# Performance work log

Measured on AMD Instinct MI355X. Metric: run time of the kernel, lower is better.

## Reference

```python
import jax, jax.numpy as jnp
import numpy as np

N_NODES = 100000
N_EDGES = 600000
D_IN = 128
D_OUT = 128


def setup_inputs() -> dict:
    key = jax.random.key(0)
    k1, k2, k3 = jax.random.split(key, 3)
    x = jax.random.normal(k1, (N_NODES, D_IN), dtype=jnp.float32)
    edge_index = jax.random.randint(k2, (2, N_EDGES), 0, N_NODES, dtype=jnp.int64)
    # Glorot-style init for the GCN weight, zero bias (PyG defaults)
    W = jax.random.normal(k3, (D_IN, D_OUT), dtype=jnp.float32) * (1.0 / np.sqrt(D_IN))
    b = jnp.zeros((D_OUT,), dtype=jnp.float32)
    return {"x": x, "edge_index": edge_index, "W": W, "b": b}


def reference(x, edge_index, W, b):
    """GCNConv: out = D^{-1/2} (A + I) D^{-1/2} (x @ W) + b."""
    n = x.shape[0]
    self_loop = jnp.arange(n, dtype=edge_index.dtype)
    src = jnp.concatenate([edge_index[0], self_loop])  # [E + N]
    dst = jnp.concatenate([edge_index[1], self_loop])

    xw = x @ W  # [N, D_OUT] dense transform before aggregation

    # symmetric normalization with self-loops
    deg = jax.ops.segment_sum(jnp.ones_like(dst, dtype=x.dtype), dst, num_segments=n)
    dinv = jnp.where(deg > 0, jax.lax.rsqrt(deg), 0.0)
    norm = dinv[src] * dinv[dst]  # [E + N]

    # gather source features, scale, scatter-add to destinations
    msgs = norm[:, None] * xw[src]  # [E + N, D_OUT]
    out = jax.ops.segment_sum(msgs, dst, num_segments=n)
    return out + b
```

## Files before the change

kernel.cpp:

```cpp
#include <hip/hip_runtime.h>
#include <hip/hip_bf16.h>
#include <stdint.h>

#define N_NODES 100000
#define N_EDGES 600000
#define D 128
#define SCAN_NBLK ((N_NODES + 255) / 256)
#define CAP 32

typedef unsigned short u16;
typedef uint32_t u32;
typedef __attribute__((ext_vector_type(8))) short bf16x8;
typedef __attribute__((ext_vector_type(4))) float f32x4;

union bfpack { bf16x8 v; u16 s[8]; };

__device__ __forceinline__ float bf2f(u16 u) {
    union { u32 i; float f; } v; v.i = ((u32)u) << 16; return v.f;
}
__device__ __forceinline__ u16 f2bf(float f) {
    union { float f; u32 i; } v; v.f = f;
    u32 lsb = (v.i >> 16) & 1u;
    return (u16)((v.i + 0x7fffu + lsb) >> 16);
}

__global__ __launch_bounds__(256) void k_init(const u32* __restrict__ xu,
                                              const int* __restrict__ ei,
                                              int* __restrict__ deg,
                                              int* __restrict__ flags) {
    int t = threadIdx.x;
    int idx = blockIdx.x * 256 + t;
    if (idx < N_NODES) deg[idx] = 0;
    if (blockIdx.x == 0) {
        __shared__ int cnt[2];
        if (t < 2) cnt[t] = 0;
        __syncthreads();
        const u32* eu = (const u32*)ei;
        int bad = 0, zc = 0;
        for (int i = 0; i < 16; i++) {
            u32 w = xu[t + 256 * i];
            int e0 = (w >> 7) & 0xFF, e1 = (w >> 23) & 0xFF;
            bad += ((e0 == 0 || e0 == 0xFF) ? 1 : 0) + ((e1 == 0 || e1 == 0xFF) ? 1 : 0);
            zc += (eu[2 * (t + 256 * i) + 1] == 0) ? 1 : 0;
        }
        atomicAdd(&cnt[0], bad);
        atomicAdd(&cnt[1], zc);
        __syncthreads();
        if (t == 0) { flags[0] = cnt[0] > 8 ? 1 : 0; flags[1] = cnt[1] > 2048 ? 1 : 0; }
    }
}

__global__ __launch_bounds__(256) void k_prep(const int* __restrict__ flags,
                                              const void* __restrict__ Wp,
                                              u16* __restrict__ wthi,
                                              u16* __restrict__ wtlo) {
    int t = blockIdx.x * 256 + threadIdx.x;
    if (flags[0]) {
        const float* Wf = (const float*)Wp;
        for (int i = 0; i < 8; i++) {
            int idx = t + i * 2048;
            float w = Wf[idx];
            int k = idx >> 7, n = idx & 127;
            u16 h = f2bf(w);
            wthi[n * 128 + k] = h;
            wtlo[n * 128 + k] = f2bf(w - bf2f(h));
        }
    } else {
        const u16* W16 = (const u16*)Wp;
        for (int i = 0; i < 8; i++) {
            int idx = t + i * 2048;
            int k = idx >> 7, n = idx & 127;
            wthi[n * 128 + k] = W16[idx];
        }
    }
}

__global__ __launch_bounds__(256) void k_build(const int* __restrict__ ei,
                                               const int* __restrict__ flags,
                                               int* __restrict__ cnt,
                                               int* __restrict__ csr) {
    int e = blockIdx.x * 256 + threadIdx.x;
    if (e >= N_EDGES) return;
    int s, d;
    if (flags[1]) { s = ei[2 * e]; d = ei[2 * (N_EDGES + e)]; }
    else          { s = ei[e];     d = ei[N_EDGES + e]; }
    if ((unsigned)s >= N_NODES) s = 0;
    if ((unsigned)d >= N_NODES) d = 0;
    int slot = atomicAdd(&cnt[d], 1);
    if (slot < CAP) csr[(long)d * CAP + slot] = s;
}

__global__ void k_hist(const int* __restrict__ ei, const int* __restrict__ flags,
                       int* __restrict__ deg) {
    int e = blockIdx.x * 256 + threadIdx.x;
    if (e < N_EDGES) {
        int d = flags[1] ? ei[2 * (N_EDGES + e)] : ei[N_EDGES + e];
        if ((unsigned)d >= N_NODES) d = 0;
        atomicAdd(&deg[d], 1);
    }
}

__global__ __launch_bounds__(256) void k_reduce(const int* __restrict__ deg,
                                                int* __restrict__ bsum) {
    __shared__ int ws[4];
    int t = threadIdx.x, lane = t & 63, wave = t >> 6;
    int idx = blockIdx.x * 256 + t;
    int v = (idx < N_NODES) ? deg[idx] : 0;
    for (int o = 32; o > 0; o >>= 1) v += __shfl_down(v, o, 64);
    if (lane == 0) ws[wave] = v;
    __syncthreads();
    if (t == 0) bsum[blockIdx.x] = ws[0] + ws[1] + ws[2] + ws[3];
}

__global__ __launch_bounds__(512) void k_scanbs(const int* __restrict__ bsum,
                                                int* __restrict__ bpre,
                                                int* __restrict__ offs) {
    __shared__ int lds[512];
    int t = threadIdx.x;
    int v = (t < SCAN_NBLK) ? bsum[t] : 0;
    lds[t] = v;
    __syncthreads();
    for (int off = 1; off < 512; off <<= 1) {
        int u = (t >= off) ? lds[t - off] : 0;
        __syncthreads();
        lds[t] += u;
        __syncthreads();
    }
    if (t < SCAN_NBLK) bpre[t] = (t == 0) ? 0 : lds[t - 1];
    if (t == SCAN_NBLK - 1) offs[N_NODES] = lds[t];
}

__global__ __launch_bounds__(256) void k_apply(const int* __restrict__ deg,
                                               const int* __restrict__ bpre,
                                               int* __restrict__ offs,
                                               int* __restrict__ cursor) {
    __shared__ int ws[4];
    int t = threadIdx.x, lane = t & 63, wave = t >> 6;
    int idx = blockIdx.x * 256 + t;
    int d = (idx < N_NODES) ? deg[idx] : 0;
    int v = d;
    for (int o = 1; o < 64; o <<= 1) {
        int u = __shfl_up(v, o, 64);
        if (lane >= o) v += u;
    }
    if (lane == 63) ws[wave] = v;
    __syncthreads();
    int add = 0;
    for (int w = 0; w < wave; w++) add += ws[w];
    int excl = bpre[blockIdx.x] + add + v - d;
    if (idx < N_NODES) {
        offs[idx] = excl;
        cursor[idx] = excl;
    }
}

__global__ void k_scatter(const int* __restrict__ ei, const int* __restrict__ flags,
                          int* __restrict__ cursor, int* __restrict__ csr) {
    int e = blockIdx.x * 256 + threadIdx.x;
    if (e < N_EDGES) {
        int s, d;
        if (flags[1]) { s = ei[2 * e]; d = ei[2 * (N_EDGES + e)]; }
        else          { s = ei[e];     d = ei[N_EDGES + e]; }
        if ((unsigned)s >= N_NODES) s = 0;
        if ((unsigned)d >= N_NODES) d = 0;
        int slot = atomicAdd(&cursor[d], 1);
        csr[slot] = s;
    }
}

__global__ __launch_bounds__(256, 2) void k_gemm(const int* __restrict__ flags,
                                                 const void* __restrict__ xp,
                                                 const u16* __restrict__ wthi,
                                                 const u16* __restrict__ wtlo,
                                                 const int* __restrict__ deg,
                                                 u16* __restrict__ xw) {
    int t = threadIdx.x, wave = t >> 6, lane = t & 63;
    int m16 = lane & 15, q = lane >> 4;
    int row0 = blockIdx.x * 128 + wave * 32;
    f32x4 acc[2][8];
    for (int a = 0; a < 2; a++)
        for (int c = 0; c < 8; c++) acc[a][c] = (f32x4){0.f, 0.f, 0.f, 0.f};

    int r0 = row0 + m16;      if (r0 > N_NODES - 1) r0 = N_NODES - 1;
    int r1 = row0 + 16 + m16; if (r1 > N_NODES - 1) r1 = N_NODES - 1;

    if (flags[0]) {
        const float* xf = (const float*)xp;
        for (int kt = 0; kt < 4; kt++) {
            int kbase = kt * 32 + q * 8;
            float4 u0 = *(const float4*)(xf + (long)r0 * D + kbase);
            float4 u1 = *(const float4*)(xf + (long)r0 * D + kbase + 4);
            float4 v0 = *(const float4*)(xf + (long)r1 * D + kbase);
            float4 v1 = *(const float4*)(xf + (long)r1 * D + kbase + 4);
            float t0[8] = {u0.x, u0.y, u0.z, u0.w, u1.x, u1.y, u1.z, u1.w};
            float t1[8] = {v0.x, v0.y, v0.z, v0.w, v1.x, v1.y, v1.z, v1.w};
            bfpack h0, l0, h1, l1;
            for (int j = 0; j < 8; j++) {
                u16 a = f2bf(t0[j]); h0.s[j] = a; l0.s[j] = f2bf(t0[j] - bf2f(a));
                u16 b = f2bf(t1[j]); h1.s[j] = b; l1.s[j] = f2bf(t1[j] - bf2f(b));
            }
            for (int ct = 0; ct < 8; ct++) {
                bf16x8 bh = *(const bf16x8*)(wthi + (ct * 16 + m16) * 128 + kbase);
                bf16x8 bl = *(const bf16x8*)(wtlo + (ct * 16 + m16) * 128 + kbase);
                acc[0][ct] = __builtin_amdgcn_mfma_f32_16x16x32_bf16(h0.v, bh, acc[0][ct], 0, 0, 0);
                acc[0][ct] = __builtin_amdgcn_mfma_f32_16x16x32_bf16(l0.v, bh, acc[0][ct], 0, 0, 0);
                acc[0][ct] = __builtin_amdgcn_mfma_f32_16x16x32_bf16(h0.v, bl, acc[0][ct], 0, 0, 0);
                acc[1][ct] = __builtin_amdgcn_mfma_f32_16x16x32_bf16(h1.v, bh, acc[1][ct], 0, 0, 0);
                acc[1][ct] = __builtin_amdgcn_mfma_f32_16x16x32_bf16(l1.v, bh, acc[1][ct], 0, 0, 0);
                acc[1][ct] = __builtin_amdgcn_mfma_f32_16x16x32_bf16(h1.v, bl, acc[1][ct], 0, 0, 0);
            }
        }
    } else {
        const u16* x16 = (const u16*)xp;
        bf16x8 wb[8][4];
#pragma unroll
        for (int ct = 0; ct < 8; ct++)
#pragma unroll
            for (int kt = 0; kt < 4; kt++)
                wb[ct][kt] = *(const bf16x8*)(wthi + (ct * 16 + m16) * 128 + kt * 32 + q * 8);
        bf16x8 a0[4], a1[4];
#pragma unroll
        for (int kt = 0; kt < 4; kt++) {
            int kbase = kt * 32 + q * 8;
            a0[kt] = *(const bf16x8*)(x16 + (long)r0 * D + kbase);
            a1[kt] = *(const bf16x8*)(x16 + (long)r1 * D + kbase);
        }
#pragma unroll
        for (int kt = 0; kt < 4; kt++)
#pragma unroll
            for (int ct = 0; ct < 8; ct++) {
                acc[0][ct] = __builtin_amdgcn_mfma_f32_16x16x32_bf16(a0[kt], wb[ct][kt], acc[0][ct], 0, 0, 0);
                acc[1][ct] = __builtin_amdgcn_mfma_f32_16x16x32_bf16(a1[kt], wb[ct][kt], acc[1][ct], 0, 0, 0);
            }
    }
    for (int a = 0; a < 2; a++)
        for (int r = 0; r < 4; r++) {
            int row = row0 + a * 16 + q * 4 + r;
            if (row < N_NODES) {
                float dr = rsqrtf((float)(deg[row] + 1));
                for (int ct = 0; ct < 8; ct++)
                    xw[(long)row * D + ct * 16 + m16] = f2bf(dr * acc[a][ct][r]);
            }
        }
}

__global__ __launch_bounds__(256) void k_agg_bkt(const int* __restrict__ flags,
                                                 const u16* __restrict__ xw,
                                                 const int* __restrict__ csr,
                                                 const int* __restrict__ cnt,
                                                 const void* __restrict__ bp,
                                                 void* __restrict__ outp) {
    int t = threadIdx.x;
    int wave = t >> 6, lane = t & 63;
    int g = lane >> 4, i = lane & 15;
    int nb = blockIdx.x * 16 + wave * 4;
    int n = nb + g;

    int4 dv = *(const int4*)(cnt + nb);
    int deg = (g == 0) ? dv.x : (g == 1) ? dv.y : (g == 2) ? dv.z : dv.w;
    float dn = rsqrtf((float)(deg + 1));
    int m = deg < CAP ? deg : CAP;
    int rounds = (m + 3) >> 2;
    float padf = (float)(1 - (rounds * 4 - m));

    const u16* xwc = xw + i * 8;
    bfpack pv; pv.v = *(const bf16x8*)(xwc + (long)n * D);
    float ax[8];
#pragma unroll
    for (int j2 = 0; j2 < 8; j2++) ax[j2] = bf2f(pv.s[j2]) * padf;

    const int* base = csr + (long)n * CAP;
    for (int j = 0; j < m; j += 4) {
        int4 qi = *(const int4*)(base + j);
        int s0 = qi.x;
        int s1 = (j + 1 < m) ? qi.y : n;
        int s2 = (j + 2 < m) ? qi.z : n;
        int s3 = (j + 3 < m) ? qi.w : n;
        bfpack g0, g1, g2, g3;
        g0.v = *(const bf16x8*)(xwc + (long)s0 * D);
        g1.v = *(const bf16x8*)(xwc + (long)s1 * D);
        g2.v = *(const bf16x8*)(xwc + (long)s2 * D);
        g3.v = *(const bf16x8*)(xwc + (long)s3 * D);
#pragma unroll
        for (int j2 = 0; j2 < 8; j2++)
            ax[j2] += (bf2f(g0.s[j2]) + bf2f(g1.s[j2])) +
                      (bf2f(g2.s[j2]) + bf2f(g3.s[j2]));
    }

    if (flags[0]) {
        const float* bf_ = (const float*)bp;
        f32x4 b0 = *(const f32x4*)(bf_ + i * 8);
        f32x4 b1 = *(const f32x4*)(bf_ + i * 8 + 4);
        f32x4 o0, o1;
#pragma unroll
        for (int j2 = 0; j2 < 4; j2++) {
            o0[j2] = dn * ax[j2] + b0[j2];
            o1[j2] = dn * ax[j2 + 4] + b1[j2];
        }
        float* outf = (float*)outp;
        *(f32x4*)(outf + (long)n * D + i * 8) = o0;
        *(f32x4*)(outf + (long)n * D + i * 8 + 4) = o1;
    } else {
        const u16* b16 = (const u16*)bp;
        bfpack bb; bb.v = *(const bf16x8*)(b16 + i * 8);
        bfpack ob;
#pragma unroll
        for (int j2 = 0; j2 < 8; j2++) ob.s[j2] = f2bf(dn * ax[j2] + bf2f(bb.s[j2]));
        u16* out16 = (u16*)outp;
        *(bf16x8*)(out16 + (long)n * D + i * 8) = ob.v;
    }
}

__global__ __launch_bounds__(256) void k_agg_csr(const int* __restrict__ flags,
                                                 const u16* __restrict__ xw,
                                                 const int* __restrict__ csr,
                                                 const int* __restrict__ offs,
                                                 const void* __restrict__ bp,
                                                 void* __restrict__ outp) {
    int wave = threadIdx.x >> 6, lane = threadIdx.x & 63;
    int n = blockIdx.x * 4 + wave;
    int c = lane * 2;
    int e0 = offs[n], e1 = offs[n + 1];
    float dn = rsqrtf((float)(e1 - e0 + 1));
    u32 pv = *(const u32*)(xw + (long)n * D + c);
    float ax = bf2f((u16)pv), ay = bf2f((u16)(pv >> 16));
    int j = e0;
    for (; j + 4 <= e1; j += 4) {
        int s0 = csr[j], s1 = csr[j + 1], s2 = csr[j + 2], s3 = csr[j + 3];
        u32 q0 = *(const u32*)(xw + (long)s0 * D + c);
        u32 q1 = *(const u32*)(xw + (long)s1 * D + c);
        u32 q2 = *(const u32*)(xw + (long)s2 * D + c);
        u32 q3 = *(const u32*)(xw + (long)s3 * D + c);
        ax += bf2f((u16)q0) + bf2f((u16)q1) + bf2f((u16)q2) + bf2f((u16)q3);
        ay += bf2f((u16)(q0 >> 16)) + bf2f((u16)(q1 >> 16)) +
              bf2f((u16)(q2 >> 16)) + bf2f((u16)(q3 >> 16));
    }
    for (; j < e1; j++) {
        int s = csr[j];
        u32 qv = *(const u32*)(xw + (long)s * D + c);
        ax += bf2f((u16)qv);
        ay += bf2f((u16)(qv >> 16));
    }
    if (flags[0]) {
        const float* bf_ = (const float*)bp;
        float2 bb = *(const float2*)(bf_ + c);
        float* outf = (float*)outp;
        *(float2*)(outf + (long)n * D + c) = make_float2(dn * ax + bb.x, dn * ay + bb.y);
    } else {
        const u16* b16 = (const u16*)bp;
        u32 bb = *(const u32*)(b16 + c);
        u16* out16 = (u16*)outp;
        u32 o = (u32)f2bf(dn * ax + bf2f((u16)bb)) |
                ((u32)f2bf(dn * ay + bf2f((u16)(bb >> 16))) << 16);
        *(u32*)(out16 + (long)n * D + c) = o;
    }
}

extern "C" void kernel_launch(void* const* d_in, const int* in_sizes, int n_in,
                              void* d_out, int out_size, void* d_ws, size_t ws_size,
                              hipStream_t stream) {
    const void* x  = d_in[0];
    const int* ei  = (const int*)d_in[1];
    const void* W  = d_in[2];
    const void* b  = d_in[3];
    char* ws = (char*)d_ws;

    const size_t BUCKET_NEED = 38865664 + 64;
    if (ws_size >= BUCKET_NEED) {
        int* flags = (int*)(ws + 0);
        int* cnt   = (int*)(ws + 64);
        int* csr   = (int*)(ws + 400128);
        u16* xw    = (u16*)(ws + 13200128);
        u16* wthi  = (u16*)(ws + 38800128);
        u16* wtlo  = (u16*)(ws + 38832896);
        k_init<<<SCAN_NBLK, 256, 0, stream>>>((const u32*)x, ei, cnt, flags);
        k_build<<<(N_EDGES + 255) / 256, 256, 0, stream>>>(ei, flags, cnt, csr);
        k_prep<<<8, 256, 0, stream>>>(flags, W, wthi, wtlo);
        k_gemm<<<(N_NODES + 127) / 128, 256, 0, stream>>>(flags, x, wthi, wtlo, cnt, xw);
        k_agg_bkt<<<N_NODES / 16, 256, 0, stream>>>(flags, xw, csr, cnt, b, d_out);
    } else {
        int*   flags  = (int*)(ws + 0);
        int*   deg    = (int*)(ws + 64);
        int*   offs   = (int*)(ws + 400064);
        int*   cursor = (int*)(ws + 800068);
        int*   csr    = (int*)(ws + 1200068);
        int*   bsum   = (int*)(ws + 3600068);
        int*   bpre   = (int*)(ws + 3601636);
        u16*   xw     = (u16*)(ws + 3603216);
        u16*   wthi   = (u16*)(ws + 29203264);
        u16*   wtlo   = (u16*)(ws + 29236032);
        k_init<<<SCAN_NBLK, 256, 0, stream>>>((const u32*)x, ei, deg, flags);
        k_hist<<<(N_EDGES + 255) / 256, 256, 0, stream>>>(ei, flags, deg);
        k_reduce<<<SCAN_NBLK, 256, 0, stream>>>(deg, bsum);
        k_scanbs<<<1, 512, 0, stream>>>(bsum, bpre, offs);
        k_apply<<<SCAN_NBLK, 256, 0, stream>>>(deg, bpre, offs, cursor);
        k_prep<<<8, 256, 0, stream>>>(flags, W, wthi, wtlo);
        k_gemm<<<(N_NODES + 127) / 128, 256, 0, stream>>>(flags, x, wthi, wtlo, deg, xw);
        k_scatter<<<(N_EDGES + 255) / 256, 256, 0, stream>>>(ei, flags, cursor, csr);
        k_agg_csr<<<N_NODES / 4, 256, 0, stream>>>(flags, xw, csr, offs, b, d_out);
    }
}
```

Baseline: 207.8 us.

## Store xw in column-group-major layout, slot-major CSR, LDS-staged W in GEMM

The GEMM now writes xw as eight 16-column slabs (each slab a [N_NODES,16] array) instead of row-major. The new aggregation kernel assigns each block to one slab, so the gather working set per slab is about 3.2MB and can stay cache-resident. The bucket CSR is stored slot-major (groups of 4 slots interleaved across nodes) so neighbour-index loads coalesce across lanes. The fp32 GEMM path stages W hi/lo halves in padded LDS and raises the occupancy hint. The cost is 32-bit scattered gathers instead of 16-byte ones, and eight passes over the edge lists.

```diff
diff --git a/kernel.cpp b/kernel.cpp
--- a/kernel.cpp
+++ b/kernel.cpp
@@ -5,6 +5,7 @@
 #define N_NODES 100000
 #define N_EDGES 600000
 #define D 128
+#define WT2 72
 #define SCAN_NBLK ((N_NODES + 255) / 256)
 #define CAP 32
 
@@ -23,6 +24,7 @@
     u32 lsb = (v.i >> 16) & 1u;
     return (u16)((v.i + 0x7fffu + lsb) >> 16);
 }
+
 
 __global__ __launch_bounds__(256) void k_init(const u32* __restrict__ xu,
                                               const int* __restrict__ ei,
@@ -87,7 +89,8 @@
     if ((unsigned)s >= N_NODES) s = 0;
     if ((unsigned)d >= N_NODES) d = 0;
     int slot = atomicAdd(&cnt[d], 1);
-    if (slot < CAP) csr[(long)d * CAP + slot] = s;
+    if (slot < CAP)
+        csr[((long)(slot >> 2) * N_NODES + d) * 4 + (slot & 3)] = s;
 }
 
 __global__ void k_hist(const int* __restrict__ ei, const int* __restrict__ flags,
@@ -168,12 +171,13 @@
     }
 }
 
-__global__ __launch_bounds__(256, 2) void k_gemm(const int* __restrict__ flags,
+__global__ __launch_bounds__(256, 3) void k_gemm(const int* __restrict__ flags,
                                                  const void* __restrict__ xp,
                                                  const u16* __restrict__ wthi,
                                                  const u16* __restrict__ wtlo,
                                                  const int* __restrict__ deg,
                                                  u16* __restrict__ xw) {
+    __shared__ u16 Wlds[2][128 * WT2];
     int t = threadIdx.x, wave = t >> 6, lane = t & 63;
     int m16 = lane & 15, q = lane >> 4;
     int row0 = blockIdx.x * 128 + wave * 32;
@@ -186,28 +190,52 @@
 
     if (flags[0]) {
         const float* xf = (const float*)xp;
-        for (int kt = 0; kt < 4; kt++) {
-            int kbase = kt * 32 + q * 8;
-            float4 u0 = *(const float4*)(xf + (long)r0 * D + kbase);
-            float4 u1 = *(const float4*)(xf + (long)r0 * D + kbase + 4);
-            float4 v0 = *(const float4*)(xf + (long)r1 * D + kbase);
-            float4 v1 = *(const float4*)(xf + (long)r1 * D + kbase + 4);
-            float t0[8] = {u0.x, u0.y, u0.z, u0.w, u1.x, u1.y, u1.z, u1.w};
-            float t1[8] = {v0.x, v0.y, v0.z, v0.w, v1.x, v1.y, v1.z, v1.w};
-            bfpack h0, l0, h1, l1;
-            for (int j = 0; j < 8; j++) {
-                u16 a = f2bf(t0[j]); h0.s[j] = a; l0.s[j] = f2bf(t0[j] - bf2f(a));
-                u16 b = f2bf(t1[j]); h1.s[j] = b; l1.s[j] = f2bf(t1[j] - bf2f(b));
+#pragma unroll
+        for (int kh = 0; kh < 2; kh++) {
+            float4 xr[8];
+#pragma unroll
+            for (int kt = 0; kt < 2; kt++) {
+                int kg = kh * 64 + kt * 32 + q * 8;
+                xr[kt * 4 + 0] = *(const float4*)(xf + (long)r0 * D + kg);
+                xr[kt * 4 + 1] = *(const float4*)(xf + (long)r0 * D + kg + 4);
+                xr[kt * 4 + 2] = *(const float4*)(xf + (long)r1 * D + kg);
+                xr[kt * 4 + 3] = *(const float4*)(xf + (long)r1 * D + kg + 4);
             }
-            for (int ct = 0; ct < 8; ct++) {
-                bf16x8 bh = *(const bf16x8*)(wthi + (ct * 16 + m16) * 128 + kbase);
-                bf16x8 bl = *(const bf16x8*)(wtlo + (ct * 16 + m16) * 128 + kbase);
-                acc[0][ct] = __builtin_amdgcn_mfma_f32_16x16x32_bf16(h0.v, bh, acc[0][ct], 0, 0, 0);
-                acc[0][ct] = __builtin_amdgcn_mfma_f32_16x16x32_bf16(l0.v, bh, acc[0][ct], 0, 0, 0);
-                acc[0][ct] = __builtin_amdgcn_mfma_f32_16x16x32_bf16(h0.v, bl, acc[0][ct], 0, 0, 0);
-                acc[1][ct] = __builtin_amdgcn_mfma_f32_16x16x32_bf16(h1.v, bh, acc[1][ct], 0, 0, 0);
-                acc[1][ct] = __builtin_amdgcn_mfma_f32_16x16x32_bf16(l1.v, bh, acc[1][ct], 0, 0, 0);
-                acc[1][ct] = __builtin_amdgcn_mfma_f32_16x16x32_bf16(h1.v, bl, acc[1][ct], 0, 0, 0);
+            if (kh) __syncthreads();
+#pragma unroll
+            for (int i = 0; i < 8; i++) {
+                int idx = i * 256 + t;
+                int arr = idx >> 10;
+                int r = (idx >> 3) & 127;
+                int c8 = idx & 7;
+                const u16* src = (arr ? wtlo : wthi) + r * 128 + kh * 64 + c8 * 8;
+                *(bf16x8*)&Wlds[arr][r * WT2 + c8 * 8] = *(const bf16x8*)src;
+            }
+            __syncthreads();
+#pragma unroll
+            for (int kt = 0; kt < 2; kt++) {
+                int kl = kt * 32 + q * 8;
+                float t0[8] = {xr[kt * 4 + 0].x, xr[kt * 4 + 0].y, xr[kt * 4 + 0].z, xr[kt * 4 + 0].w,
+                               xr[kt * 4 + 1].x, xr[kt * 4 + 1].y, xr[kt * 4 + 1].z, xr[kt * 4 + 1].w};
+                float t1[8] = {xr[kt * 4 + 2].x, xr[kt * 4 + 2].y, xr[kt * 4 + 2].z, xr[kt * 4 + 2].w,
+                               xr[kt * 4 + 3].x, xr[kt * 4 + 3].y, xr[kt * 4 + 3].z, xr[kt * 4 + 3].w};
+                bfpack h0, l0, h1, l1;
+#pragma unroll
+                for (int j = 0; j < 8; j++) {
+                    u16 a = f2bf(t0[j]); h0.s[j] = a; l0.s[j] = f2bf(t0[j] - bf2f(a));
+                    u16 b = f2bf(t1[j]); h1.s[j] = b; l1.s[j] = f2bf(t1[j] - bf2f(b));
+                }
+#pragma unroll
+                for (int ct = 0; ct < 8; ct++) {
+                    bf16x8 bh = *(const bf16x8*)(&Wlds[0][(ct * 16 + m16) * WT2 + kl]);
+                    bf16x8 bl = *(const bf16x8*)(&Wlds[1][(ct * 16 + m16) * WT2 + kl]);
+                    acc[0][ct] = __builtin_amdgcn_mfma_f32_16x16x32_bf16(h0.v, bh, acc[0][ct], 0, 0, 0);
+                    acc[0][ct] = __builtin_amdgcn_mfma_f32_16x16x32_bf16(l0.v, bh, acc[0][ct], 0, 0, 0);
+                    acc[0][ct] = __builtin_amdgcn_mfma_f32_16x16x32_bf16(h0.v, bl, acc[0][ct], 0, 0, 0);
+                    acc[1][ct] = __builtin_amdgcn_mfma_f32_16x16x32_bf16(h1.v, bh, acc[1][ct], 0, 0, 0);
+                    acc[1][ct] = __builtin_amdgcn_mfma_f32_16x16x32_bf16(l1.v, bh, acc[1][ct], 0, 0, 0);
+                    acc[1][ct] = __builtin_amdgcn_mfma_f32_16x16x32_bf16(h1.v, bl, acc[1][ct], 0, 0, 0);
+                }
             }
         }
     } else {
@@ -239,80 +267,67 @@
             if (row < N_NODES) {
                 float dr = rsqrtf((float)(deg[row] + 1));
                 for (int ct = 0; ct < 8; ct++)
-                    xw[(long)row * D + ct * 16 + m16] = f2bf(dr * acc[a][ct][r]);
+                    xw[((long)ct * N_NODES + row) * 16 + m16] = f2bf(dr * acc[a][ct][r]);
             }
         }
 }
 
-__global__ __launch_bounds__(256) void k_agg_bkt(const int* __restrict__ flags,
-                                                 const u16* __restrict__ xw,
-                                                 const int* __restrict__ csr,
-                                                 const int* __restrict__ cnt,
-                                                 const void* __restrict__ bp,
-                                                 void* __restrict__ outp) {
+__global__ __launch_bounds__(256) void k_agg2(const int* __restrict__ flags,
+                                              const u16* __restrict__ xws,
+                                              const int* __restrict__ csr,
+                                              const int* __restrict__ cnt,
+                                              const void* __restrict__ bp,
+                                              void* __restrict__ outp) {
     int t = threadIdx.x;
     int wave = t >> 6, lane = t & 63;
-    int g = lane >> 4, i = lane & 15;
-    int nb = blockIdx.x * 16 + wave * 4;
-    int n = nb + g;
-
-    int4 dv = *(const int4*)(cnt + nb);
-    int deg = (g == 0) ? dv.x : (g == 1) ? dv.y : (g == 2) ? dv.z : dv.w;
+    int g2 = lane >> 3;
+    int il = lane & 7;
+    int grp = blockIdx.x & 7;
+    int n = (blockIdx.x >> 3) * 32 + wave * 8 + g2;
+
+    int deg = cnt[n];
     float dn = rsqrtf((float)(deg + 1));
     int m = deg < CAP ? deg : CAP;
     int rounds = (m + 3) >> 2;
     float padf = (float)(1 - (rounds * 4 - m));
 
-    const u16* xwc = xw + i * 8;
-    bfpack pv; pv.v = *(const bf16x8*)(xwc + (long)n * D);
-    float ax[8];
-#pragma unroll
-    for (int j2 = 0; j2 < 8; j2++) ax[j2] = bf2f(pv.s[j2]) * padf;
-
-    const int* base = csr + (long)n * CAP;
+    const u16* xc = xws + (long)grp * N_NODES * 16 + il * 2;
+    u32 pv = *(const u32*)(xc + (long)n * 16);
+    float ax = bf2f((u16)pv) * padf, ay = bf2f((u16)(pv >> 16)) * padf;
+
     for (int j = 0; j < m; j += 4) {
-        int4 qi = *(const int4*)(base + j);
+        int4 qi = *(const int4*)(csr + ((long)(j >> 2) * N_NODES + n) * 4);
         int s0 = qi.x;
         int s1 = (j + 1 < m) ? qi.y : n;
         int s2 = (j + 2 < m) ? qi.z : n;
         int s3 = (j + 3 < m) ? qi.w : n;
-        bfpack g0, g1, g2, g3;
-        g0.v = *(const bf16x8*)(xwc + (long)s0 * D);
-        g1.v = *(const bf16x8*)(xwc + (long)s1 * D);
-        g2.v = *(const bf16x8*)(xwc + (long)s2 * D);
-        g3.v = *(const bf16x8*)(xwc + (long)s3 * D);
-#pragma unroll
-        for (int j2 = 0; j2 < 8; j2++)
-            ax[j2] += (bf2f(g0.s[j2]) + bf2f(g1.s[j2])) +
-                      (bf2f(g2.s[j2]) + bf2f(g3.s[j2]));
-    }
-
+        u32 v0 = *(const u32*)(xc + (long)s0 * 16);
+        u32 v1 = *(const u32*)(xc + (long)s1 * 16);
+        u32 v2 = *(const u32*)(xc + (long)s2 * 16);
+        u32 v3 = *(const u32*)(xc + (long)s3 * 16);
+        ax += (bf2f((u16)v0) + bf2f((u16)v1)) + (bf2f((u16)v2) + bf2f((u16)v3));
+        ay += (bf2f((u16)(v0 >> 16)) + bf2f((u16)(v1 >> 16))) +
+              (bf2f((u16)(v2 >> 16)) + bf2f((u16)(v3 >> 16)));
+    }
+
+    int c0 = grp * 16 + il * 2;
     if (flags[0]) {
         const float* bf_ = (const float*)bp;
-        f32x4 b0 = *(const f32x4*)(bf_ + i * 8);
-        f32x4 b1 = *(const f32x4*)(bf_ + i * 8 + 4);
-        f32x4 o0, o1;
-#pragma unroll
-        for (int j2 = 0; j2 < 4; j2++) {
-            o0[j2] = dn * ax[j2] + b0[j2];
-            o1[j2] = dn * ax[j2 + 4] + b1[j2];
-        }
+        float2 bb = *(const float2*)(bf_ + c0);
         float* outf = (float*)outp;
-        *(f32x4*)(outf + (long)n * D + i * 8) = o0;
-        *(f32x4*)(outf + (long)n * D + i * 8 + 4) = o1;
+        *(float2*)(outf + (long)n * D + c0) = make_float2(dn * ax + bb.x, dn * ay + bb.y);
     } else {
         const u16* b16 = (const u16*)bp;
-        bfpack bb; bb.v = *(const bf16x8*)(b16 + i * 8);
-        bfpack ob;
-#pragma unroll
-        for (int j2 = 0; j2 < 8; j2++) ob.s[j2] = f2bf(dn * ax[j2] + bf2f(bb.s[j2]));
+        u32 bb = *(const u32*)(b16 + c0);
         u16* out16 = (u16*)outp;
-        *(bf16x8*)(out16 + (long)n * D + i * 8) = ob.v;
+        u32 o = (u32)f2bf(dn * ax + bf2f((u16)bb)) |
+                ((u32)f2bf(dn * ay + bf2f((u16)(bb >> 16))) << 16);
+        *(u32*)(out16 + (long)n * D + c0) = o;
     }
 }
 
 __global__ __launch_bounds__(256) void k_agg_csr(const int* __restrict__ flags,
-                                                 const u16* __restrict__ xw,
+                                                 const u16* __restrict__ xws,
                                                  const int* __restrict__ csr,
                                                  const int* __restrict__ offs,
                                                  const void* __restrict__ bp,
@@ -320,24 +335,25 @@
     int wave = threadIdx.x >> 6, lane = threadIdx.x & 63;
     int n = blockIdx.x * 4 + wave;
     int c = lane * 2;
+    const u16* xc = xws + (long)(lane >> 3) * N_NODES * 16 + (c & 15);
     int e0 = offs[n], e1 = offs[n + 1];
     float dn = rsqrtf((float)(e1 - e0 + 1));
-    u32 pv = *(const u32*)(xw + (long)n * D + c);
+    u32 pv = *(const u32*)(xc + (long)n * 16);
     float ax = bf2f((u16)pv), ay = bf2f((u16)(pv >> 16));
     int j = e0;
     for (; j + 4 <= e1; j += 4) {
         int s0 = csr[j], s1 = csr[j + 1], s2 = csr[j + 2], s3 = csr[j + 3];
-        u32 q0 = *(const u32*)(xw + (long)s0 * D + c);
-        u32 q1 = *(const u32*)(xw + (long)s1 * D + c);
-        u32 q2 = *(const u32*)(xw + (long)s2 * D + c);
-        u32 q3 = *(const u32*)(xw + (long)s3 * D + c);
+        u32 q0 = *(const u32*)(xc + (long)s0 * 16);
+        u32 q1 = *(const u32*)(xc + (long)s1 * 16);
+        u32 q2 = *(const u32*)(xc + (long)s2 * 16);
+        u32 q3 = *(const u32*)(xc + (long)s3 * 16);
         ax += bf2f((u16)q0) + bf2f((u16)q1) + bf2f((u16)q2) + bf2f((u16)q3);
         ay += bf2f((u16)(q0 >> 16)) + bf2f((u16)(q1 >> 16)) +
               bf2f((u16)(q2 >> 16)) + bf2f((u16)(q3 >> 16));
     }
     for (; j < e1; j++) {
         int s = csr[j];
-        u32 qv = *(const u32*)(xw + (long)s * D + c);
+        u32 qv = *(const u32*)(xc + (long)s * 16);
         ax += bf2f((u16)qv);
         ay += bf2f((u16)(qv >> 16));
     }
@@ -377,7 +393,7 @@
         k_build<<<(N_EDGES + 255) / 256, 256, 0, stream>>>(ei, flags, cnt, csr);
         k_prep<<<8, 256, 0, stream>>>(flags, W, wthi, wtlo);
         k_gemm<<<(N_NODES + 127) / 128, 256, 0, stream>>>(flags, x, wthi, wtlo, cnt, xw);
-        k_agg_bkt<<<N_NODES / 16, 256, 0, stream>>>(flags, xw, csr, cnt, b, d_out);
+        k_agg2<<<8 * (N_NODES / 32), 256, 0, stream>>>(flags, xw, csr, cnt, b, d_out);
     } else {
         int*   flags  = (int*)(ws + 0);
         int*   deg    = (int*)(ws + 64);
```

New measurement: 202.4 us. 2.6% less time.

## Interleave CSR buckets by slot group, stage W in LDS, prefetch eight neighbors

Applied to the files above, without the earlier changes.

The fixed-capacity neighbor buckets are stored slot-group-major, so groups of four slots for consecutive nodes sit next to each other. This makes the aggregation's index loads coalesced across the wave. The aggregation kernel now issues the first eight neighbor gathers up front, padding with self-loops, to raise memory-level parallelism for the typical degree of about six. The fp32 GEMM path stages the hi/lo bf16 weight halves into LDS in two K halves and raises the occupancy hint to 3, at the cost of extra barriers and LDS usage.

```diff
diff --git a/kernel.cpp b/kernel.cpp
--- a/kernel.cpp
+++ b/kernel.cpp
@@ -5,6 +5,7 @@
 #define N_NODES 100000
 #define N_EDGES 600000
 #define D 128
+#define WT2 72
 #define SCAN_NBLK ((N_NODES + 255) / 256)
 #define CAP 32
 
@@ -23,6 +24,7 @@
     u32 lsb = (v.i >> 16) & 1u;
     return (u16)((v.i + 0x7fffu + lsb) >> 16);
 }
+
 
 __global__ __launch_bounds__(256) void k_init(const u32* __restrict__ xu,
                                               const int* __restrict__ ei,
@@ -87,7 +89,8 @@
     if ((unsigned)s >= N_NODES) s = 0;
     if ((unsigned)d >= N_NODES) d = 0;
     int slot = atomicAdd(&cnt[d], 1);
-    if (slot < CAP) csr[(long)d * CAP + slot] = s;
+    if (slot < CAP)
+        csr[((long)(slot >> 2) * N_NODES + d) * 4 + (slot & 3)] = s;
 }
 
 __global__ void k_hist(const int* __restrict__ ei, const int* __restrict__ flags,
@@ -168,12 +171,13 @@
     }
 }
 
-__global__ __launch_bounds__(256, 2) void k_gemm(const int* __restrict__ flags,
+__global__ __launch_bounds__(256, 3) void k_gemm(const int* __restrict__ flags,
                                                  const void* __restrict__ xp,
                                                  const u16* __restrict__ wthi,
                                                  const u16* __restrict__ wtlo,
                                                  const int* __restrict__ deg,
                                                  u16* __restrict__ xw) {
+    __shared__ u16 Wlds[2][128 * WT2];
     int t = threadIdx.x, wave = t >> 6, lane = t & 63;
     int m16 = lane & 15, q = lane >> 4;
     int row0 = blockIdx.x * 128 + wave * 32;
@@ -186,28 +190,52 @@
 
     if (flags[0]) {
         const float* xf = (const float*)xp;
-        for (int kt = 0; kt < 4; kt++) {
-            int kbase = kt * 32 + q * 8;
-            float4 u0 = *(const float4*)(xf + (long)r0 * D + kbase);
-            float4 u1 = *(const float4*)(xf + (long)r0 * D + kbase + 4);
-            float4 v0 = *(const float4*)(xf + (long)r1 * D + kbase);
-            float4 v1 = *(const float4*)(xf + (long)r1 * D + kbase + 4);
-            float t0[8] = {u0.x, u0.y, u0.z, u0.w, u1.x, u1.y, u1.z, u1.w};
-            float t1[8] = {v0.x, v0.y, v0.z, v0.w, v1.x, v1.y, v1.z, v1.w};
-            bfpack h0, l0, h1, l1;
-            for (int j = 0; j < 8; j++) {
-                u16 a = f2bf(t0[j]); h0.s[j] = a; l0.s[j] = f2bf(t0[j] - bf2f(a));
-                u16 b = f2bf(t1[j]); h1.s[j] = b; l1.s[j] = f2bf(t1[j] - bf2f(b));
+#pragma unroll
+        for (int kh = 0; kh < 2; kh++) {
+            float4 xr[8];
+#pragma unroll
+            for (int kt = 0; kt < 2; kt++) {
+                int kg = kh * 64 + kt * 32 + q * 8;
+                xr[kt * 4 + 0] = *(const float4*)(xf + (long)r0 * D + kg);
+                xr[kt * 4 + 1] = *(const float4*)(xf + (long)r0 * D + kg + 4);
+                xr[kt * 4 + 2] = *(const float4*)(xf + (long)r1 * D + kg);
+                xr[kt * 4 + 3] = *(const float4*)(xf + (long)r1 * D + kg + 4);
             }
-            for (int ct = 0; ct < 8; ct++) {
-                bf16x8 bh = *(const bf16x8*)(wthi + (ct * 16 + m16) * 128 + kbase);
-                bf16x8 bl = *(const bf16x8*)(wtlo + (ct * 16 + m16) * 128 + kbase);
-                acc[0][ct] = __builtin_amdgcn_mfma_f32_16x16x32_bf16(h0.v, bh, acc[0][ct], 0, 0, 0);
-                acc[0][ct] = __builtin_amdgcn_mfma_f32_16x16x32_bf16(l0.v, bh, acc[0][ct], 0, 0, 0);
-                acc[0][ct] = __builtin_amdgcn_mfma_f32_16x16x32_bf16(h0.v, bl, acc[0][ct], 0, 0, 0);
-                acc[1][ct] = __builtin_amdgcn_mfma_f32_16x16x32_bf16(h1.v, bh, acc[1][ct], 0, 0, 0);
-                acc[1][ct] = __builtin_amdgcn_mfma_f32_16x16x32_bf16(l1.v, bh, acc[1][ct], 0, 0, 0);
-                acc[1][ct] = __builtin_amdgcn_mfma_f32_16x16x32_bf16(h1.v, bl, acc[1][ct], 0, 0, 0);
+            if (kh) __syncthreads();
+#pragma unroll
+            for (int i = 0; i < 8; i++) {
+                int idx = i * 256 + t;
+                int arr = idx >> 10;
+                int r = (idx >> 3) & 127;
+                int c8 = idx & 7;
+                const u16* src = (arr ? wtlo : wthi) + r * 128 + kh * 64 + c8 * 8;
+                *(bf16x8*)&Wlds[arr][r * WT2 + c8 * 8] = *(const bf16x8*)src;
+            }
+            __syncthreads();
+#pragma unroll
+            for (int kt = 0; kt < 2; kt++) {
+                int kl = kt * 32 + q * 8;
+                float t0[8] = {xr[kt * 4 + 0].x, xr[kt * 4 + 0].y, xr[kt * 4 + 0].z, xr[kt * 4 + 0].w,
+                               xr[kt * 4 + 1].x, xr[kt * 4 + 1].y, xr[kt * 4 + 1].z, xr[kt * 4 + 1].w};
+                float t1[8] = {xr[kt * 4 + 2].x, xr[kt * 4 + 2].y, xr[kt * 4 + 2].z, xr[kt * 4 + 2].w,
+                               xr[kt * 4 + 3].x, xr[kt * 4 + 3].y, xr[kt * 4 + 3].z, xr[kt * 4 + 3].w};
+                bfpack h0, l0, h1, l1;
+#pragma unroll
+                for (int j = 0; j < 8; j++) {
+                    u16 a = f2bf(t0[j]); h0.s[j] = a; l0.s[j] = f2bf(t0[j] - bf2f(a));
+                    u16 b = f2bf(t1[j]); h1.s[j] = b; l1.s[j] = f2bf(t1[j] - bf2f(b));
+                }
+#pragma unroll
+                for (int ct = 0; ct < 8; ct++) {
+                    bf16x8 bh = *(const bf16x8*)(&Wlds[0][(ct * 16 + m16) * WT2 + kl]);
+                    bf16x8 bl = *(const bf16x8*)(&Wlds[1][(ct * 16 + m16) * WT2 + kl]);
+                    acc[0][ct] = __builtin_amdgcn_mfma_f32_16x16x32_bf16(h0.v, bh, acc[0][ct], 0, 0, 0);
+                    acc[0][ct] = __builtin_amdgcn_mfma_f32_16x16x32_bf16(l0.v, bh, acc[0][ct], 0, 0, 0);
+                    acc[0][ct] = __builtin_amdgcn_mfma_f32_16x16x32_bf16(h0.v, bl, acc[0][ct], 0, 0, 0);
+                    acc[1][ct] = __builtin_amdgcn_mfma_f32_16x16x32_bf16(h1.v, bh, acc[1][ct], 0, 0, 0);
+                    acc[1][ct] = __builtin_amdgcn_mfma_f32_16x16x32_bf16(l1.v, bh, acc[1][ct], 0, 0, 0);
+                    acc[1][ct] = __builtin_amdgcn_mfma_f32_16x16x32_bf16(h1.v, bl, acc[1][ct], 0, 0, 0);
+                }
             }
         }
     } else {
@@ -260,31 +288,51 @@
     int deg = (g == 0) ? dv.x : (g == 1) ? dv.y : (g == 2) ? dv.z : dv.w;
     float dn = rsqrtf((float)(deg + 1));
     int m = deg < CAP ? deg : CAP;
-    int rounds = (m + 3) >> 2;
-    float padf = (float)(1 - (rounds * 4 - m));
+    int P = (m <= 8) ? 8 : ((m + 3) & ~3);
+    float padf = (float)(1 - (P - m));
 
     const u16* xwc = xw + i * 8;
+    int4 q0 = *(const int4*)(csr + (long)n * 4);
+    int4 q1 = *(const int4*)(csr + ((long)N_NODES + n) * 4);
     bfpack pv; pv.v = *(const bf16x8*)(xwc + (long)n * D);
+
+    int s0 = (0 < m) ? q0.x : n, s1 = (1 < m) ? q0.y : n;
+    int s2 = (2 < m) ? q0.z : n, s3 = (3 < m) ? q0.w : n;
+    int s4 = (4 < m) ? q1.x : n, s5 = (5 < m) ? q1.y : n;
+    int s6 = (6 < m) ? q1.z : n, s7 = (7 < m) ? q1.w : n;
+    bfpack g0, g1, g2, g3, g4, g5, g6, g7;
+    g0.v = *(const bf16x8*)(xwc + (long)s0 * D);
+    g1.v = *(const bf16x8*)(xwc + (long)s1 * D);
+    g2.v = *(const bf16x8*)(xwc + (long)s2 * D);
+    g3.v = *(const bf16x8*)(xwc + (long)s3 * D);
+    g4.v = *(const bf16x8*)(xwc + (long)s4 * D);
+    g5.v = *(const bf16x8*)(xwc + (long)s5 * D);
+    g6.v = *(const bf16x8*)(xwc + (long)s6 * D);
+    g7.v = *(const bf16x8*)(xwc + (long)s7 * D);
+
     float ax[8];
 #pragma unroll
-    for (int j2 = 0; j2 < 8; j2++) ax[j2] = bf2f(pv.s[j2]) * padf;
-
-    const int* base = csr + (long)n * CAP;
-    for (int j = 0; j < m; j += 4) {
-        int4 qi = *(const int4*)(base + j);
-        int s0 = qi.x;
-        int s1 = (j + 1 < m) ? qi.y : n;
-        int s2 = (j + 2 < m) ? qi.z : n;
-        int s3 = (j + 3 < m) ? qi.w : n;
-        bfpack g0, g1, g2, g3;
-        g0.v = *(const bf16x8*)(xwc + (long)s0 * D);
-        g1.v = *(const bf16x8*)(xwc + (long)s1 * D);
-        g2.v = *(const bf16x8*)(xwc + (long)s2 * D);
-        g3.v = *(const bf16x8*)(xwc + (long)s3 * D);
+    for (int j2 = 0; j2 < 8; j2++) {
+        ax[j2] = bf2f(pv.s[j2]) * padf +
+                 ((bf2f(g0.s[j2]) + bf2f(g1.s[j2])) + (bf2f(g2.s[j2]) + bf2f(g3.s[j2]))) +
+                 ((bf2f(g4.s[j2]) + bf2f(g5.s[j2])) + (bf2f(g6.s[j2]) + bf2f(g7.s[j2])));
+    }
+
+    for (int j = 8; j < m; j += 4) {
+        int4 qi = *(const int4*)(csr + ((long)(j >> 2) * N_NODES + n) * 4);
+        int t0 = qi.x;
+        int t1 = (j + 1 < m) ? qi.y : n;
+        int t2 = (j + 2 < m) ? qi.z : n;
+        int t3 = (j + 3 < m) ? qi.w : n;
+        bfpack h0, h1, h2, h3;
+        h0.v = *(const bf16x8*)(xwc + (long)t0 * D);
+        h1.v = *(const bf16x8*)(xwc + (long)t1 * D);
+        h2.v = *(const bf16x8*)(xwc + (long)t2 * D);
+        h3.v = *(const bf16x8*)(xwc + (long)t3 * D);
 #pragma unroll
         for (int j2 = 0; j2 < 8; j2++)
-            ax[j2] += (bf2f(g0.s[j2]) + bf2f(g1.s[j2])) +
-                      (bf2f(g2.s[j2]) + bf2f(g3.s[j2]));
+            ax[j2] += (bf2f(h0.s[j2]) + bf2f(h1.s[j2])) +
+                      (bf2f(h2.s[j2]) + bf2f(h3.s[j2]));
     }
 
     if (flags[0]) {
```

After: 186.6 us. -10.2%, faster.
